# Kernel optimization log

Measured on AMD Instinct MI355X. Metric: run time of the kernel, lower is better.

## Reference

```python
import jax, jax.numpy as jnp
import numpy as np

B, S, D, H = 4, 1024, 1024, 16
HD = D // H  # head dim 64
EPS = 1e-12

def setup_inputs() -> dict:
    key = jax.random.key(0)
    ks = jax.random.split(key, 10)
    sc = 1.0 / np.sqrt(D)
    return {
        "eeg": jax.random.normal(ks[0], (B, S, D), jnp.float32),
        "pic": jax.random.normal(ks[1], (B, S, D), jnp.float32),
        "Wk": jax.random.normal(ks[2], (D, D), jnp.float32) * sc,
        "bk": jnp.zeros((D,), jnp.float32),
        "Wq": jax.random.normal(ks[3], (D, D), jnp.float32) * sc,
        "bq": jnp.zeros((D,), jnp.float32),
        "Wv": jax.random.normal(ks[4], (D, D), jnp.float32) * sc,
        "bv": jnp.zeros((D,), jnp.float32),
        "Wd": jax.random.normal(ks[5], (D, D), jnp.float32) * sc,
        "bd": jnp.zeros((D,), jnp.float32),
        "ln_w": jnp.ones((D,), jnp.float32),
        "ln_b": jnp.zeros((D,), jnp.float32),
    }

def _heads(x):  # [B,S,D] -> [B,H,S,HD]
    return x.reshape(B, S, H, HD).transpose(0, 2, 1, 3)

def reference(eeg, pic, Wk, bk, Wq, bq, Wv, bv, Wd, bd, ln_w, ln_b):
    k = _heads(eeg @ Wk + bk)
    q = _heads(pic @ Wq + bq)
    v = _heads(pic @ Wv + bv)
    scores = jnp.einsum('bhqd,bhkd->bhqk', q, k) / jnp.sqrt(jnp.float32(HD))
    probs = jax.nn.softmax(scores, axis=-1)  # dropout = identity (eval mode)
    ctx = jnp.einsum('bhqk,bhkd->bhqd', probs, v)
    ctx = ctx.transpose(0, 2, 1, 3).reshape(B, S, D)
    h = ctx @ Wd + bd  # out_dropout = identity (eval)
    x = h + pic
    u = x.mean(-1, keepdims=True)
    s = ((x - u) ** 2).mean(-1, keepdims=True)
    x = (x - u) / jnp.sqrt(s + EPS)
    return ln_w * x + ln_b
```

## Files before the change

kernel.cpp:

```cpp
#include <hip/hip_runtime.h>
#include <hip/hip_bf16.h>

#define BB 4
#define SS 1024
#define DD 1024
#define HH 16
#define HD 64
#define MM (BB * SS)
#define LN_EPS 1e-12f

typedef unsigned short u16;
typedef __attribute__((ext_vector_type(8))) short bf16x8;
typedef __attribute__((ext_vector_type(4))) float f32x4;
typedef __attribute__((ext_vector_type(4))) unsigned short u16x4;
typedef __attribute__((ext_vector_type(8))) unsigned short u16x8;

__device__ __forceinline__ u16 f2bf(float f) {
    unsigned u; __builtin_memcpy(&u, &f, 4);
    unsigned r = (u + 0x7fffu + ((u >> 16) & 1u)) >> 16;
    return (u16)r;
}
__device__ __forceinline__ float bf2f(u16 u) {
    unsigned v = ((unsigned)u) << 16;
    float f; __builtin_memcpy(&f, &v, 4); return f;
}

typedef const __attribute__((address_space(1))) unsigned int* gas1_t;
typedef __attribute__((address_space(3))) unsigned int* las3_t;
__device__ __forceinline__ void gload16(const void* g, void* s) {
    __builtin_amdgcn_global_load_lds((gas1_t)g, (las3_t)s, 16, 0, 0);
}

__global__ __launch_bounds__(256) void conv2_bf16(
    const float* __restrict__ a, const float* __restrict__ c,
    u16* __restrict__ oa, u16* __restrict__ oc)
{
    const float* in = blockIdx.y ? c : a;
    u16* out = blockIdx.y ? oc : oa;
    size_t i = ((size_t)blockIdx.x * 256 + threadIdx.x) * 8;
    float4 x = *(const float4*)(in + i);
    float4 y = *(const float4*)(in + i + 4);
    u16x8 o;
    o[0]=f2bf(x.x); o[1]=f2bf(x.y); o[2]=f2bf(x.z); o[3]=f2bf(x.w);
    o[4]=f2bf(y.x); o[5]=f2bf(y.y); o[6]=f2bf(y.z); o[7]=f2bf(y.w);
    *(u16x8*)(out + i) = o;
}

__global__ __launch_bounds__(256) void transpose_w4(
    const float* __restrict__ W0, const float* __restrict__ W1,
    const float* __restrict__ W2, const float* __restrict__ W3,
    u16* __restrict__ T0, u16* __restrict__ T1,
    u16* __restrict__ T2, u16* __restrict__ T3)
{
    const int z = blockIdx.z;
    const float* W = (z==0)?W0:(z==1)?W1:(z==2)?W2:W3;
    u16* Wt = (z==0)?T0:(z==1)?T1:(z==2)?T2:T3;

    __shared__ float Ls[64][65];
    const int t = threadIdx.x;
    const int k0 = blockIdx.x * 64, n0 = blockIdx.y * 64;
    #pragma unroll
    for (int i = 0; i < 4; ++i) {
        int r = (t >> 4) + i * 16, c = (t & 15) * 4;
        float4 v = *(const float4*)&W[(size_t)(k0 + r) * DD + n0 + c];
        Ls[r][c] = v.x; Ls[r][c+1] = v.y; Ls[r][c+2] = v.z; Ls[r][c+3] = v.w;
    }
    __syncthreads();
    #pragma unroll
    for (int i = 0; i < 2; ++i) {
        int n = (t >> 3) + i * 32, kc = (t & 7) * 8;
        u16x8 o;
        #pragma unroll
        for (int j = 0; j < 8; ++j) o[j] = f2bf(Ls[kc + j][n]);
        *(u16x8*)&Wt[(size_t)(n0 + n) * DD + k0 + kc] = o;
    }
}

__device__ __forceinline__ void gemm_mainloop(
    const u16* __restrict__ A, const u16* __restrict__ Bt,
    int bm, int bn, u16* As, u16* Bs, f32x4 (&acc)[4][2])
{
    const int tid = threadIdx.x;
    const int w = tid >> 6, l = tid & 63, g = l >> 4, lr = l & 15;
    const int wm = w >> 1, wn = w & 1;

    for (int k0 = 0; k0 < DD; k0 += 64) {
        #pragma unroll
        for (int rr = 0; rr < 4; ++rr) {
            int Cc = rr * 256 + tid;
            int row = Cc >> 3, s = Cc & 7, gc = s ^ (row & 7);
            gload16(A + (size_t)(bm + row) * DD + k0 + gc * 8,
                    As + (rr * 256 + w * 64) * 8);
        }
        #pragma unroll
        for (int rr = 0; rr < 2; ++rr) {
            int Cc = rr * 256 + tid;
            int row = Cc >> 3, s = Cc & 7, gc = s ^ (row & 7);
            gload16(Bt + (size_t)(bn + row) * DD + k0 + gc * 8,
                    Bs + (rr * 256 + w * 64) * 8);
        }
        __syncthreads();

        #pragma unroll
        for (int kh = 0; kh < 2; ++kh) {
            bf16x8 af[4], bfr[2];
            #pragma unroll
            for (int mi = 0; mi < 4; ++mi) {
                int row = wm * 64 + mi * 16 + lr;
                af[mi] = *(const bf16x8*)((const char*)As + row * 128 +
                                          ((kh * 4 + g) ^ (row & 7)) * 16);
            }
            #pragma unroll
            for (int ni = 0; ni < 2; ++ni) {
                int row = wn * 32 + ni * 16 + lr;
                bfr[ni] = *(const bf16x8*)((const char*)Bs + row * 128 +
                                           ((kh * 4 + g) ^ (row & 7)) * 16);
            }
            #pragma unroll
            for (int mi = 0; mi < 4; ++mi)
                #pragma unroll
                for (int ni = 0; ni < 2; ++ni)
                    acc[mi][ni] = __builtin_amdgcn_mfma_f32_16x16x32_bf16(
                        af[mi], bfr[ni], acc[mi][ni], 0, 0, 0);
        }
        __syncthreads();
    }
}

__global__ __launch_bounds__(256) void gemm_qkv(
    const u16* __restrict__ Ae, const u16* __restrict__ Ap,
    const u16* __restrict__ Bk, const u16* __restrict__ Bq, const u16* __restrict__ Bv,
    const float* __restrict__ bk, const float* __restrict__ bq, const float* __restrict__ bv,
    u16* __restrict__ Kb, u16* __restrict__ Qb, u16* __restrict__ VtG)
{
    const int sel = blockIdx.y >> 4;
    const int bn = (blockIdx.y & 15) * 64;
    const int bm = blockIdx.x * 128;
    const u16* A  = sel ? Ap : Ae;
    const u16* Bt = (sel == 0) ? Bk : (sel == 1) ? Bq : Bv;
    const float* bias = (sel == 0) ? bk : (sel == 1) ? bq : bv;
    const float alpha = (sel == 1) ? 0.180336880111120f : 1.0f;

    __shared__ u16 As[128 * 64];
    __shared__ u16 Bs[64 * 64];

    f32x4 acc[4][2];
    #pragma unroll
    for (int mi = 0; mi < 4; ++mi)
        #pragma unroll
        for (int ni = 0; ni < 2; ++ni) { f32x4 z = {0,0,0,0}; acc[mi][ni] = z; }

    gemm_mainloop(A, Bt, bm, bn, As, Bs, acc);

    const int tid = threadIdx.x;
    const int w = tid >> 6, l = tid & 63, g = l >> 4, lr = l & 15;
    const int wm = w >> 1, wn = w & 1;
    float bvv[2];
    bvv[0] = bias[bn + wn * 32 + lr];
    bvv[1] = bias[bn + wn * 32 + 16 + lr];

    if (sel == 2) {
        #pragma unroll
        for (int mi = 0; mi < 4; ++mi)
            #pragma unroll
            for (int ni = 0; ni < 2; ++ni) {
                int col = bn + wn * 32 + ni * 16 + lr;
                int row0 = bm + wm * 64 + mi * 16 + g * 4;
                u16x4 o;
                #pragma unroll
                for (int r = 0; r < 4; ++r) o[r] = f2bf(acc[mi][ni][r] + bvv[ni]);
                *(u16x4*)&VtG[(size_t)col * MM + row0] = o;
            }
    } else {
        u16* C = sel ? Qb : Kb;
        #pragma unroll
        for (int mi = 0; mi < 4; ++mi)
            #pragma unroll
            for (int ni = 0; ni < 2; ++ni)
                #pragma unroll
                for (int r = 0; r < 4; ++r) {
                    int row = bm + wm * 64 + mi * 16 + g * 4 + r;
                    int col = bn + wn * 32 + ni * 16 + lr;
                    C[(size_t)row * DD + col] = f2bf(alpha * (acc[mi][ni][r] + bvv[ni]));
                }
    }
}

__global__ __launch_bounds__(256) void gemm_plain(
    const u16* __restrict__ A, const u16* __restrict__ Bt,
    const float* __restrict__ bias, u16* __restrict__ C)
{
    const int bm = blockIdx.x * 128, bn = blockIdx.y * 64;
    __shared__ u16 As[128 * 64];
    __shared__ u16 Bs[64 * 64];

    f32x4 acc[4][2];
    #pragma unroll
    for (int mi = 0; mi < 4; ++mi)
        #pragma unroll
        for (int ni = 0; ni < 2; ++ni) { f32x4 z = {0,0,0,0}; acc[mi][ni] = z; }

    gemm_mainloop(A, Bt, bm, bn, As, Bs, acc);

    const int tid = threadIdx.x;
    const int w = tid >> 6, l = tid & 63, g = l >> 4, lr = l & 15;
    const int wm = w >> 1, wn = w & 1;
    float bvv[2];
    bvv[0] = bias[bn + wn * 32 + lr];
    bvv[1] = bias[bn + wn * 32 + 16 + lr];
    #pragma unroll
    for (int mi = 0; mi < 4; ++mi)
        #pragma unroll
        for (int ni = 0; ni < 2; ++ni)
            #pragma unroll
            for (int r = 0; r < 4; ++r) {
                int row = bm + wm * 64 + mi * 16 + g * 4 + r;
                int col = bn + wn * 32 + ni * 16 + lr;
                C[(size_t)row * DD + col] = f2bf(acc[mi][ni][r] + bvv[ni]);
            }
}

__global__ __launch_bounds__(256) void attn_mfma(
    const u16* __restrict__ Q, const u16* __restrict__ K,
    const u16* __restrict__ Vt, u16* __restrict__ O)
{
    const int tid = threadIdx.x;
    const int w = tid >> 6, l = tid & 63, g = l >> 4, lr = l & 15;
    int bid = (int)blockIdx.x;
    bid = (bid & 7) * 128 + (bid >> 3);
    const int qb = bid & 15, h = (bid >> 4) & 15, b = bid >> 8;
    const size_t qrow0 = (size_t)b * SS + qb * 64;
    const size_t kv0 = (size_t)b * SS;
    const int hc = h * HD;

    __shared__ __align__(16) u16 Ks[64 * 64];
    __shared__ __align__(16) u16 Vs[64 * 64];
    __shared__ __align__(16) u16 Ps[4][16 * 72];

    bf16x8 qf[2];
    {
        const u16* qp = Q + (qrow0 + w * 16 + lr) * DD + hc + g * 8;
        qf[0] = *(const bf16x8*)(qp);
        qf[1] = *(const bf16x8*)(qp + 32);
    }

    f32x4 acc[4];
    #pragma unroll
    for (int dt = 0; dt < 4; ++dt) { f32x4 z = {0,0,0,0}; acc[dt] = z; }
    float m_run = -1e30f, l_run = 0.f;

    for (int kb = 0; kb < SS / 64; ++kb) {
        #pragma unroll
        for (int rr = 0; rr < 2; ++rr) {
            int Cc = rr * 256 + tid;
            int row = Cc >> 3, s = Cc & 7, gc = s ^ (row & 7);
            gload16(K + (kv0 + kb * 64 + row) * DD + hc + gc * 8,
                    Ks + (rr * 256 + w * 64) * 8);
        }
        #pragma unroll
        for (int rr = 0; rr < 2; ++rr) {
            int Cc = rr * 256 + tid;
            int row = Cc >> 3, s = Cc & 7, gc = s ^ (row & 7);
            gload16(Vt + (size_t)(hc + row) * MM + kv0 + kb * 64 + gc * 8,
                    Vs + (rr * 256 + w * 64) * 8);
        }
        __syncthreads();

        f32x4 st[4];
        #pragma unroll
        for (int kt = 0; kt < 4; ++kt) {
            int row = kt * 16 + lr;
            const char* rb = (const char*)Ks + row * 128;
            bf16x8 k0 = *(const bf16x8*)(rb + ((0 + g) ^ (row & 7)) * 16);
            bf16x8 k1 = *(const bf16x8*)(rb + ((4 + g) ^ (row & 7)) * 16);
            f32x4 z = {0,0,0,0};
            z = __builtin_amdgcn_mfma_f32_16x16x32_bf16(k0, qf[0], z, 0, 0, 0);
            z = __builtin_amdgcn_mfma_f32_16x16x32_bf16(k1, qf[1], z, 0, 0, 0);
            st[kt] = z;
        }

        float tmax = -1e30f;
        #pragma unroll
        for (int kt = 0; kt < 4; ++kt)
            #pragma unroll
            for (int r = 0; r < 4; ++r) tmax = fmaxf(tmax, st[kt][r]);
        tmax = fmaxf(tmax, __shfl_xor(tmax, 16));
        tmax = fmaxf(tmax, __shfl_xor(tmax, 32));

        if (!__all(tmax <= m_run + 8.f)) {
            float m_new = fmaxf(m_run, tmax);
            float sc = exp2f(m_run - m_new);
            m_run = m_new;
            l_run *= sc;
            float scq[4];
            #pragma unroll
            for (int r = 0; r < 4; ++r) scq[r] = __shfl(sc, g * 4 + r);
            #pragma unroll
            for (int dt = 0; dt < 4; ++dt)
                #pragma unroll
                for (int r = 0; r < 4; ++r) acc[dt][r] *= scq[r];
        }

        float p[16];
        float ps = 0.f;
        #pragma unroll
        for (int kt = 0; kt < 4; ++kt)
            #pragma unroll
            for (int r = 0; r < 4; ++r) {
                float v = exp2f(st[kt][r] - m_run);
                p[kt * 4 + r] = v;
                ps += v;
            }
        ps += __shfl_xor(ps, 16);
        ps += __shfl_xor(ps, 32);
        l_run += ps;

        #pragma unroll
        for (int kt = 0; kt < 4; ++kt) {
            u16x4 h4;
            #pragma unroll
            for (int r = 0; r < 4; ++r) h4[r] = f2bf(p[kt * 4 + r]);
            *(u16x4*)((char*)&Ps[w][0] + lr * 144 + kt * 32 + g * 8) = h4;
        }

        #pragma unroll
        for (int kh = 0; kh < 2; ++kh) {
            bf16x8 pf = *(const bf16x8*)((const char*)&Ps[w][0] + lr * 144 +
                                         kh * 64 + g * 16);
            #pragma unroll
            for (int dt = 0; dt < 4; ++dt) {
                int row = dt * 16 + lr;
                bf16x8 vf = *(const bf16x8*)((const char*)Vs + row * 128 +
                                             ((kh * 4 + g) ^ (row & 7)) * 16);
                acc[dt] = __builtin_amdgcn_mfma_f32_16x16x32_bf16(pf, vf, acc[dt], 0, 0, 0);
            }
        }
        __syncthreads();
    }

    float invl[4];
    #pragma unroll
    for (int r = 0; r < 4; ++r) invl[r] = 1.f / __shfl(l_run, g * 4 + r);
    #pragma unroll
    for (int dt = 0; dt < 4; ++dt)
        #pragma unroll
        for (int r = 0; r < 4; ++r) {
            size_t row = qrow0 + w * 16 + g * 4 + r;
            O[row * DD + hc + dt * 16 + lr] = f2bf(acc[dt][r] * invl[r]);
        }
}

__global__ __launch_bounds__(256) void ln_kernel(
    const u16* __restrict__ Hs, const float* __restrict__ P,
    const float* __restrict__ w, const float* __restrict__ bshift,
    float* __restrict__ out)
{
    const int row = blockIdx.x;
    const int tid = threadIdx.x;
    const size_t off = (size_t)row * DD;
    const int c0 = tid * 4;

    u16x4 h4 = *(const u16x4*)&Hs[off + c0];
    float4 p4 = *(const float4*)&P[off + c0];
    float x[4];
    x[0] = bf2f(h4[0]) + p4.x; x[1] = bf2f(h4[1]) + p4.y;
    x[2] = bf2f(h4[2]) + p4.z; x[3] = bf2f(h4[3]) + p4.w;

    float s = x[0] + x[1] + x[2] + x[3];
    #pragma unroll
    for (int o = 32; o >= 1; o >>= 1) s += __shfl_xor(s, o, 64);

    __shared__ float r1[4], r2[4];
    const int wid = tid >> 6;
    if ((tid & 63) == 0) r1[wid] = s;
    __syncthreads();
    const float mean = (r1[0] + r1[1] + r1[2] + r1[3]) * (1.f / (float)DD);

    float d2 = 0.f;
    #pragma unroll
    for (int i = 0; i < 4; ++i) { float d = x[i] - mean; d2 += d * d; }
    #pragma unroll
    for (int o = 32; o >= 1; o >>= 1) d2 += __shfl_xor(d2, o, 64);
    if ((tid & 63) == 0) r2[wid] = d2;
    __syncthreads();
    const float var = (r2[0] + r2[1] + r2[2] + r2[3]) * (1.f / (float)DD);
    const float inv = rsqrtf(var + LN_EPS);

    float4 o4;
    o4.x = w[c0 + 0] * ((x[0] - mean) * inv) + bshift[c0 + 0];
    o4.y = w[c0 + 1] * ((x[1] - mean) * inv) + bshift[c0 + 1];
    o4.z = w[c0 + 2] * ((x[2] - mean) * inv) + bshift[c0 + 2];
    o4.w = w[c0 + 3] * ((x[3] - mean) * inv) + bshift[c0 + 3];
    *(float4*)&out[off + c0] = o4;
}

extern "C" void kernel_launch(void* const* d_in, const int* in_sizes, int n_in,
                              void* d_out, int out_size, void* d_ws, size_t ws_size,
                              hipStream_t stream)
{
    const float* eeg = (const float*)d_in[0];
    const float* pic = (const float*)d_in[1];
    const float* Wk  = (const float*)d_in[2];
    const float* bk  = (const float*)d_in[3];
    const float* Wq  = (const float*)d_in[4];
    const float* bq  = (const float*)d_in[5];
    const float* Wv  = (const float*)d_in[6];
    const float* bv  = (const float*)d_in[7];
    const float* Wd  = (const float*)d_in[8];
    const float* bd  = (const float*)d_in[9];
    const float* lnw = (const float*)d_in[10];
    const float* lnb = (const float*)d_in[11];
    float* out = (float*)d_out;

    u16* ws = (u16*)d_ws;
    const size_t M4 = (size_t)1 << 22;
    u16* Ae  = ws;
    u16* Ap  = ws + M4;
    u16* WtK = ws + 2 * M4;
    u16* WtQ = WtK + (1u << 20);
    u16* WtV = WtQ + (1u << 20);
    u16* WtD = WtV + (1u << 20);
    u16* Kb  = ws + 3 * M4;
    u16* Qb  = ws + 4 * M4;
    u16* VtG = ws + 5 * M4;
    u16* Cb  = ws + 6 * M4;
    u16* Hb  = ws + 7 * M4;

    conv2_bf16<<<dim3(2048, 2), 256, 0, stream>>>(eeg, pic, Ae, Ap);
    transpose_w4<<<dim3(16, 16, 4), 256, 0, stream>>>(Wk, Wq, Wv, Wd,
                                                      WtK, WtQ, WtV, WtD);

    gemm_qkv<<<dim3(32, 48), 256, 0, stream>>>(Ae, Ap, WtK, WtQ, WtV,
                                               bk, bq, bv, Kb, Qb, VtG);

    attn_mfma<<<BB * HH * (SS / 64), 256, 0, stream>>>(Qb, Kb, VtG, Cb);

    gemm_plain<<<dim3(32, 16), 256, 0, stream>>>(Cb, WtD, bd, Hb);

    ln_kernel<<<MM, 256, 0, stream>>>(Hb, pic, lnw, lnb, out);
}
```

Baseline: 122.1 us.

## Enlarge GEMM tiles to 128x128, double-buffer attention K/V, use 512-thread attention blocks

The QKV and output-projection GEMMs move from 128x64 to 128x128 tiles with a swizzled block order for L2 locality. The V projection now swaps MFMA operands so the transposed store is produced directly. Attention uses 512-thread blocks covering 128 query rows, double-buffers K/V tiles in LDS so the next tile loads while the current one computes, and adds s_setprio around the MFMA sections. The goals are better operand reuse, fewer LDS/global round trips and hidden load latency, at the cost of more registers and fewer blocks in the grid.

```diff
diff --git a/kernel.cpp b/kernel.cpp
--- a/kernel.cpp
+++ b/kernel.cpp
@@ -16,9 +16,8 @@
 typedef __attribute__((ext_vector_type(8))) unsigned short u16x8;
 
 __device__ __forceinline__ u16 f2bf(float f) {
-    unsigned u; __builtin_memcpy(&u, &f, 4);
-    unsigned r = (u + 0x7fffu + ((u >> 16) & 1u)) >> 16;
-    return (u16)r;
+    __hip_bfloat16 h = __float2bfloat16(f);
+    u16 r; __builtin_memcpy(&r, &h, 2); return r;
 }
 __device__ __forceinline__ float bf2f(u16 u) {
     unsigned v = ((unsigned)u) << 16;
@@ -76,9 +75,10 @@
     }
 }
 
-__device__ __forceinline__ void gemm_mainloop(
+template<int TRANS>
+__device__ __forceinline__ void gemm128_loop(
     const u16* __restrict__ A, const u16* __restrict__ Bt,
-    int bm, int bn, u16* As, u16* Bs, f32x4 (&acc)[4][2])
+    int bm, int bn, u16* As, u16* Bs, f32x4 (&acc)[4][4])
 {
     const int tid = threadIdx.x;
     const int w = tid >> 6, l = tid & 63, g = l >> 4, lr = l & 15;
@@ -88,14 +88,14 @@
         #pragma unroll
         for (int rr = 0; rr < 4; ++rr) {
             int Cc = rr * 256 + tid;
-            int row = Cc >> 3, s = Cc & 7, gc = s ^ (row & 7);
+            int row = Cc >> 3, s2 = Cc & 7, gc = s2 ^ (row & 7);
             gload16(A + (size_t)(bm + row) * DD + k0 + gc * 8,
                     As + (rr * 256 + w * 64) * 8);
         }
         #pragma unroll
-        for (int rr = 0; rr < 2; ++rr) {
+        for (int rr = 0; rr < 4; ++rr) {
             int Cc = rr * 256 + tid;
-            int row = Cc >> 3, s = Cc & 7, gc = s ^ (row & 7);
+            int row = Cc >> 3, s2 = Cc & 7, gc = s2 ^ (row & 7);
             gload16(Bt + (size_t)(bn + row) * DD + k0 + gc * 8,
                     Bs + (rr * 256 + w * 64) * 8);
         }
@@ -103,7 +103,7 @@
 
         #pragma unroll
         for (int kh = 0; kh < 2; ++kh) {
-            bf16x8 af[4], bfr[2];
+            bf16x8 af[4], bfr[4];
             #pragma unroll
             for (int mi = 0; mi < 4; ++mi) {
                 int row = wm * 64 + mi * 16 + lr;
@@ -111,17 +111,22 @@
                                           ((kh * 4 + g) ^ (row & 7)) * 16);
             }
             #pragma unroll
-            for (int ni = 0; ni < 2; ++ni) {
-                int row = wn * 32 + ni * 16 + lr;
+            for (int ni = 0; ni < 4; ++ni) {
+                int row = wn * 64 + ni * 16 + lr;
                 bfr[ni] = *(const bf16x8*)((const char*)Bs + row * 128 +
                                            ((kh * 4 + g) ^ (row & 7)) * 16);
             }
             #pragma unroll
             for (int mi = 0; mi < 4; ++mi)
                 #pragma unroll
-                for (int ni = 0; ni < 2; ++ni)
-                    acc[mi][ni] = __builtin_amdgcn_mfma_f32_16x16x32_bf16(
-                        af[mi], bfr[ni], acc[mi][ni], 0, 0, 0);
+                for (int ni = 0; ni < 4; ++ni) {
+                    if (TRANS)
+                        acc[ni][mi] = __builtin_amdgcn_mfma_f32_16x16x32_bf16(
+                            bfr[ni], af[mi], acc[ni][mi], 0, 0, 0);
+                    else
+                        acc[mi][ni] = __builtin_amdgcn_mfma_f32_16x16x32_bf16(
+                            af[mi], bfr[ni], acc[mi][ni], 0, 0, 0);
+                }
         }
         __syncthreads();
     }
@@ -133,55 +138,59 @@
     const float* __restrict__ bk, const float* __restrict__ bq, const float* __restrict__ bv,
     u16* __restrict__ Kb, u16* __restrict__ Qb, u16* __restrict__ VtG)
 {
-    const int sel = blockIdx.y >> 4;
-    const int bn = (blockIdx.y & 15) * 64;
-    const int bm = blockIdx.x * 128;
+    const int sel = blockIdx.y;
+    int x = (int)blockIdx.x;
+    int sw = (x & 7) * 32 + (x >> 3);
+    const int bm = (sw & 31) * 128;
+    const int bn = (sw >> 5) * 128;
+
     const u16* A  = sel ? Ap : Ae;
     const u16* Bt = (sel == 0) ? Bk : (sel == 1) ? Bq : Bv;
     const float* bias = (sel == 0) ? bk : (sel == 1) ? bq : bv;
     const float alpha = (sel == 1) ? 0.180336880111120f : 1.0f;
 
-    __shared__ u16 As[128 * 64];
-    __shared__ u16 Bs[64 * 64];
-
-    f32x4 acc[4][2];
-    #pragma unroll
-    for (int mi = 0; mi < 4; ++mi)
-        #pragma unroll
-        for (int ni = 0; ni < 2; ++ni) { f32x4 z = {0,0,0,0}; acc[mi][ni] = z; }
-
-    gemm_mainloop(A, Bt, bm, bn, As, Bs, acc);
+    __shared__ __align__(16) u16 As[128 * 64];
+    __shared__ __align__(16) u16 Bs[128 * 64];
+
+    f32x4 acc[4][4];
+    #pragma unroll
+    for (int i = 0; i < 4; ++i)
+        #pragma unroll
+        for (int j = 0; j < 4; ++j) { f32x4 z = {0,0,0,0}; acc[i][j] = z; }
 
     const int tid = threadIdx.x;
     const int w = tid >> 6, l = tid & 63, g = l >> 4, lr = l & 15;
     const int wm = w >> 1, wn = w & 1;
-    float bvv[2];
-    bvv[0] = bias[bn + wn * 32 + lr];
-    bvv[1] = bias[bn + wn * 32 + 16 + lr];
 
     if (sel == 2) {
+        gemm128_loop<1>(A, Bt, bm, bn, As, Bs, acc);
+        #pragma unroll
+        for (int ni = 0; ni < 4; ++ni)
+            #pragma unroll
+            for (int r = 0; r < 4; ++r) {
+                int n = bn + wn * 64 + ni * 16 + g * 4 + r;
+                float bb = bias[n];
+                #pragma unroll
+                for (int mi = 0; mi < 4; ++mi) {
+                    int m = bm + wm * 64 + mi * 16 + lr;
+                    VtG[(size_t)n * MM + m] = f2bf(acc[ni][mi][r] + bb);
+                }
+            }
+    } else {
+        gemm128_loop<0>(A, Bt, bm, bn, As, Bs, acc);
+        u16* C = sel ? Qb : Kb;
+        float b4[4];
+        #pragma unroll
+        for (int ni = 0; ni < 4; ++ni) b4[ni] = bias[bn + wn * 64 + ni * 16 + lr];
         #pragma unroll
         for (int mi = 0; mi < 4; ++mi)
             #pragma unroll
-            for (int ni = 0; ni < 2; ++ni) {
-                int col = bn + wn * 32 + ni * 16 + lr;
-                int row0 = bm + wm * 64 + mi * 16 + g * 4;
-                u16x4 o;
-                #pragma unroll
-                for (int r = 0; r < 4; ++r) o[r] = f2bf(acc[mi][ni][r] + bvv[ni]);
-                *(u16x4*)&VtG[(size_t)col * MM + row0] = o;
-            }
-    } else {
-        u16* C = sel ? Qb : Kb;
-        #pragma unroll
-        for (int mi = 0; mi < 4; ++mi)
-            #pragma unroll
-            for (int ni = 0; ni < 2; ++ni)
+            for (int ni = 0; ni < 4; ++ni)
                 #pragma unroll
                 for (int r = 0; r < 4; ++r) {
                     int row = bm + wm * 64 + mi * 16 + g * 4 + r;
-                    int col = bn + wn * 32 + ni * 16 + lr;
-                    C[(size_t)row * DD + col] = f2bf(alpha * (acc[mi][ni][r] + bvv[ni]));
+                    int col = bn + wn * 64 + ni * 16 + lr;
+                    C[(size_t)row * DD + col] = f2bf(alpha * (acc[mi][ni][r] + b4[ni]));
                 }
     }
 }
@@ -190,52 +199,61 @@
     const u16* __restrict__ A, const u16* __restrict__ Bt,
     const float* __restrict__ bias, u16* __restrict__ C)
 {
-    const int bm = blockIdx.x * 128, bn = blockIdx.y * 64;
-    __shared__ u16 As[128 * 64];
-    __shared__ u16 Bs[64 * 64];
-
-    f32x4 acc[4][2];
-    #pragma unroll
-    for (int mi = 0; mi < 4; ++mi)
-        #pragma unroll
-        for (int ni = 0; ni < 2; ++ni) { f32x4 z = {0,0,0,0}; acc[mi][ni] = z; }
-
-    gemm_mainloop(A, Bt, bm, bn, As, Bs, acc);
+    int x = (int)blockIdx.x;
+    int sw = (x & 7) * 32 + (x >> 3);
+    const int bm = (sw & 31) * 128;
+    const int bn = (sw >> 5) * 128;
+
+    __shared__ __align__(16) u16 As[128 * 64];
+    __shared__ __align__(16) u16 Bs[128 * 64];
+
+    f32x4 acc[4][4];
+    #pragma unroll
+    for (int i = 0; i < 4; ++i)
+        #pragma unroll
+        for (int j = 0; j < 4; ++j) { f32x4 z = {0,0,0,0}; acc[i][j] = z; }
+
+    gemm128_loop<0>(A, Bt, bm, bn, As, Bs, acc);
 
     const int tid = threadIdx.x;
     const int w = tid >> 6, l = tid & 63, g = l >> 4, lr = l & 15;
     const int wm = w >> 1, wn = w & 1;
-    float bvv[2];
-    bvv[0] = bias[bn + wn * 32 + lr];
-    bvv[1] = bias[bn + wn * 32 + 16 + lr];
+    float b4[4];
+    #pragma unroll
+    for (int ni = 0; ni < 4; ++ni) b4[ni] = bias[bn + wn * 64 + ni * 16 + lr];
     #pragma unroll
     for (int mi = 0; mi < 4; ++mi)
         #pragma unroll
-        for (int ni = 0; ni < 2; ++ni)
+        for (int ni = 0; ni < 4; ++ni)
             #pragma unroll
             for (int r = 0; r < 4; ++r) {
                 int row = bm + wm * 64 + mi * 16 + g * 4 + r;
-                int col = bn + wn * 32 + ni * 16 + lr;
-                C[(size_t)row * DD + col] = f2bf(acc[mi][ni][r] + bvv[ni]);
-            }
-}
-
-__global__ __launch_bounds__(256) void attn_mfma(
+                int col = bn + wn * 64 + ni * 16 + lr;
+                C[(size_t)row * DD + col] = f2bf(acc[mi][ni][r] + b4[ni]);
+            }
+}
+
+__global__ __launch_bounds__(512) void attn_mfma(
     const u16* __restrict__ Q, const u16* __restrict__ K,
     const u16* __restrict__ Vt, u16* __restrict__ O)
 {
     const int tid = threadIdx.x;
     const int w = tid >> 6, l = tid & 63, g = l >> 4, lr = l & 15;
     int bid = (int)blockIdx.x;
-    bid = (bid & 7) * 128 + (bid >> 3);
-    const int qb = bid & 15, h = (bid >> 4) & 15, b = bid >> 8;
-    const size_t qrow0 = (size_t)b * SS + qb * 64;
+    bid = (bid & 7) * 64 + (bid >> 3);
+    const int qb = bid & 7, h = (bid >> 3) & 15, b = bid >> 7;
+    const size_t qrow0 = (size_t)b * SS + qb * 128;
     const size_t kv0 = (size_t)b * SS;
     const int hc = h * HD;
 
-    __shared__ __align__(16) u16 Ks[64 * 64];
-    __shared__ __align__(16) u16 Vs[64 * 64];
-    __shared__ __align__(16) u16 Ps[4][16 * 72];
+    __shared__ __align__(16) u16 Ks[2][64 * 64];
+    __shared__ __align__(16) u16 Vs[2][64 * 64];
+    __shared__ __align__(16) u16 Ps[8][16 * 72];
+
+    const int srow = tid >> 3, ss = tid & 7;
+    const int sgc = ss ^ (srow & 7);
+    const u16* kg = K + (kv0 + srow) * DD + hc + sgc * 8;
+    const u16* vg = Vt + (size_t)(hc + srow) * MM + kv0 + sgc * 8;
 
     bf16x8 qf[2];
     {
@@ -249,28 +267,25 @@
     for (int dt = 0; dt < 4; ++dt) { f32x4 z = {0,0,0,0}; acc[dt] = z; }
     float m_run = -1e30f, l_run = 0.f;
 
+    gload16(kg, &Ks[0][w * 512]);
+    gload16(vg, &Vs[0][w * 512]);
+    __syncthreads();
+
     for (int kb = 0; kb < SS / 64; ++kb) {
-        #pragma unroll
-        for (int rr = 0; rr < 2; ++rr) {
-            int Cc = rr * 256 + tid;
-            int row = Cc >> 3, s = Cc & 7, gc = s ^ (row & 7);
-            gload16(K + (kv0 + kb * 64 + row) * DD + hc + gc * 8,
-                    Ks + (rr * 256 + w * 64) * 8);
-        }
-        #pragma unroll
-        for (int rr = 0; rr < 2; ++rr) {
-            int Cc = rr * 256 + tid;
-            int row = Cc >> 3, s = Cc & 7, gc = s ^ (row & 7);
-            gload16(Vt + (size_t)(hc + row) * MM + kv0 + kb * 64 + gc * 8,
-                    Vs + (rr * 256 + w * 64) * 8);
-        }
-        __syncthreads();
+        const int cur = kb & 1;
+        if (kb < SS / 64 - 1) {
+            gload16(kg + (size_t)(kb + 1) * 64 * DD, &Ks[cur ^ 1][w * 512]);
+            gload16(vg + (size_t)(kb + 1) * 64, &Vs[cur ^ 1][w * 512]);
+        }
+        const char* kbase = (const char*)&Ks[cur][0];
+        const char* vbase = (const char*)&Vs[cur][0];
 
         f32x4 st[4];
+        __builtin_amdgcn_s_setprio(1);
         #pragma unroll
         for (int kt = 0; kt < 4; ++kt) {
             int row = kt * 16 + lr;
-            const char* rb = (const char*)Ks + row * 128;
+            const char* rb = kbase + row * 128;
             bf16x8 k0 = *(const bf16x8*)(rb + ((0 + g) ^ (row & 7)) * 16);
             bf16x8 k1 = *(const bf16x8*)(rb + ((4 + g) ^ (row & 7)) * 16);
             f32x4 z = {0,0,0,0};
@@ -278,6 +293,7 @@
             z = __builtin_amdgcn_mfma_f32_16x16x32_bf16(k1, qf[1], z, 0, 0, 0);
             st[kt] = z;
         }
+        __builtin_amdgcn_s_setprio(0);
 
         float tmax = -1e30f;
         #pragma unroll
@@ -323,6 +339,7 @@
             *(u16x4*)((char*)&Ps[w][0] + lr * 144 + kt * 32 + g * 8) = h4;
         }
 
+        __builtin_amdgcn_s_setprio(1);
         #pragma unroll
         for (int kh = 0; kh < 2; ++kh) {
             bf16x8 pf = *(const bf16x8*)((const char*)&Ps[w][0] + lr * 144 +
@@ -330,11 +347,13 @@
             #pragma unroll
             for (int dt = 0; dt < 4; ++dt) {
                 int row = dt * 16 + lr;
-                bf16x8 vf = *(const bf16x8*)((const char*)Vs + row * 128 +
+                bf16x8 vf = *(const bf16x8*)(vbase + row * 128 +
                                              ((kh * 4 + g) ^ (row & 7)) * 16);
                 acc[dt] = __builtin_amdgcn_mfma_f32_16x16x32_bf16(pf, vf, acc[dt], 0, 0, 0);
             }
         }
+        __builtin_amdgcn_s_setprio(0);
+
         __syncthreads();
     }
 
@@ -430,12 +449,12 @@
     transpose_w4<<<dim3(16, 16, 4), 256, 0, stream>>>(Wk, Wq, Wv, Wd,
                                                       WtK, WtQ, WtV, WtD);
 
-    gemm_qkv<<<dim3(32, 48), 256, 0, stream>>>(Ae, Ap, WtK, WtQ, WtV,
+    gemm_qkv<<<dim3(256, 3), 256, 0, stream>>>(Ae, Ap, WtK, WtQ, WtV,
                                                bk, bq, bv, Kb, Qb, VtG);
 
-    attn_mfma<<<BB * HH * (SS / 64), 256, 0, stream>>>(Qb, Kb, VtG, Cb);
-
-    gemm_plain<<<dim3(32, 16), 256, 0, stream>>>(Cb, WtD, bd, Hb);
+    attn_mfma<<<BB * HH * (SS / 128), 512, 0, stream>>>(Qb, Kb, VtG, Cb);
+
+    gemm_plain<<<256, 256, 0, stream>>>(Cb, WtD, bd, Hb);
 
     ln_kernel<<<MM, 256, 0, stream>>>(Hb, pic, lnw, lnb, out);
 }
```

Result: slower. 129.7 us (+6.2%).
